# Kernel optimization log

Hardware: AMD Instinct MI355X
Metric: run time of the kernel (lower is better)

Reference implementation:

```python
import jax, jax.numpy as jnp
import numpy as np

B = 2097152
CXR, ECG, EHR = 15, 14, 13
TOTAL = CXR + ECG + EHR  # 42
LN_EPS = 1e-5


def setup_inputs() -> dict:
    key = jax.random.key(0)
    ks = jax.random.split(key, 40)
    f32 = jnp.float32
    inp = {
        "cxr_probs": jax.random.normal(ks[0], (B, CXR), dtype=f32),
        "ecg_probs": jax.random.normal(ks[1], (B, ECG), dtype=f32),
        "ehr_probs": jax.random.normal(ks[2], (B, EHR), dtype=f32),
    }
    for i, (name, E) in enumerate([("cxr", CXR), ("ecg", ECG), ("ehr", EHR)]):
        k0 = 3 + i * 8
        s_in = 1.0 / np.sqrt(E)
        s_kv = 1.0 / np.sqrt(TOTAL)
        inp[f"in_w_{name}"] = jax.random.normal(ks[k0], (3 * E, E), dtype=f32) * s_in
        inp[f"in_b_{name}"] = jnp.zeros((3 * E,), dtype=f32)
        inp[f"out_w_{name}"] = jax.random.normal(ks[k0 + 1], (E, E), dtype=f32) * s_in
        inp[f"out_b_{name}"] = jnp.zeros((E,), dtype=f32)
        inp[f"kv_w_{name}"] = jax.random.normal(ks[k0 + 2], (E, TOTAL), dtype=f32) * s_kv
        inp[f"kv_b_{name}"] = jax.random.normal(ks[k0 + 3], (E,), dtype=f32) * s_kv
        inp[f"ln_g_{name}"] = jnp.ones((E,), dtype=f32)
        inp[f"ln_b_{name}"] = jnp.zeros((E,), dtype=f32)
    return inp


def _branch(x, ctx, in_w, in_b, out_w, out_b, kv_w, kv_b, ln_g, ln_b):
    # x: [B, E], ctx: [B, 42]
    E = x.shape[-1]
    kv = ctx @ kv_w.T + kv_b                      # [B, E]
    # nn.MultiheadAttention with q_len = kv_len = 1: softmax over a single
    # key is identically 1, so attn_out == v_proj(kv) exactly.
    Wv, bv = in_w[2 * E:], in_b[2 * E:]
    v = kv @ Wv.T + bv                            # [B, E]
    attended = v @ out_w.T + out_b                # [B, E]
    y = x + attended
    mu = jnp.mean(y, axis=-1, keepdims=True)
    var = jnp.mean(jnp.square(y - mu), axis=-1, keepdims=True)
    return (y - mu) * jax.lax.rsqrt(var + LN_EPS) * ln_g + ln_b


def reference(cxr_probs, ecg_probs, ehr_probs,
              in_w_cxr, in_b_cxr, out_w_cxr, out_b_cxr, kv_w_cxr, kv_b_cxr, ln_g_cxr, ln_b_cxr,
              in_w_ecg, in_b_ecg, out_w_ecg, out_b_ecg, kv_w_ecg, kv_b_ecg, ln_g_ecg, ln_b_ecg,
              in_w_ehr, in_b_ehr, out_w_ehr, out_b_ehr, kv_w_ehr, kv_b_ehr, ln_g_ehr, ln_b_ehr):
    ctx = jnp.concatenate([cxr_probs, ecg_probs, ehr_probs], axis=1)  # [B, 42]
    cxr_out = _branch(cxr_probs, ctx, in_w_cxr, in_b_cxr, out_w_cxr, out_b_cxr,
                      kv_w_cxr, kv_b_cxr, ln_g_cxr, ln_b_cxr)
    ecg_out = _branch(ecg_probs, ctx, in_w_ecg, in_b_ecg, out_w_ecg, out_b_ecg,
                      kv_w_ecg, kv_b_ecg, ln_g_ecg, ln_b_ecg)
    ehr_out = _branch(ehr_probs, ctx, in_w_ehr, in_b_ehr, out_w_ehr, out_b_ehr,
                      kv_w_ehr, kv_b_ehr, ln_g_ehr, ln_b_ehr)
    return (cxr_out, ecg_out, ehr_out)
```

## Files before the change

### kernel.cpp

```cpp
#include <hip/hip_runtime.h>
#include <stdint.h>

constexpr int CXR = 15, ECG = 14, EHR = 13;
constexpr int TOTAL = 42;
constexpr int MPITCH = 44;
constexpr float LN_EPS = 1e-5f;

constexpr int WS_M    = 0;
constexpr int WS_B    = TOTAL * MPITCH;
constexpr int WS_G    = WS_B + TOTAL;
constexpr int WS_BETA = WS_G + TOTAL;
constexpr int WS_FRAG = 1976;

constexpr int WROWS = 64;
constexpr int ARENA_B = 11264;
constexpr int S0F = 0, S1F = WROWS * CXR, S2F = S1F + WROWS * ECG;
constexpr int WC0 = WROWS * CXR / 4, WC1 = WROWS * ECG / 4, WC2 = WROWS * EHR / 4;

typedef _Float16 half8 __attribute__((ext_vector_type(8)));
typedef float float4v __attribute__((ext_vector_type(4)));
typedef __attribute__((address_space(4))) const float CFc;
__device__ __forceinline__ CFc* cast1(const float* p) {
    return (CFc*)(unsigned long long)p;
}

struct FuseArgs {
    const float *in_w, *in_b, *out_w, *out_b, *kv_w, *kv_b, *ln_g, *ln_b;
    int E, R;
};

__global__ void fuse_weights_kernel(FuseArgs a0, FuseArgs a1, FuseArgs a2,
                                    float* __restrict__ ws) {
    FuseArgs a = (blockIdx.x == 0) ? a0 : (blockIdx.x == 1 ? a1 : a2);
    const int E = a.E, R = a.R;
    const int tid = threadIdx.x;

    __shared__ float T1[15 * 42];
    __shared__ float b1[15];

    for (int idx = tid; idx < E * TOTAL; idx += blockDim.x) {
        int i = idx / TOTAL, j = idx % TOTAL;
        float acc = 0.f;
        for (int k = 0; k < E; ++k)
            acc = fmaf(a.in_w[(2 * E + i) * E + k], a.kv_w[k * TOTAL + j], acc);
        T1[i * TOTAL + j] = acc;
    }
    if (tid < E) {
        float acc = a.in_b[2 * E + tid];
        for (int k = 0; k < E; ++k)
            acc = fmaf(a.in_w[(2 * E + tid) * E + k], a.kv_b[k], acc);
        b1[tid] = acc;
    }
    __syncthreads();

    for (int idx = tid; idx < E * MPITCH; idx += blockDim.x) {
        int i = idx / MPITCH, j = idx % MPITCH;
        float acc = 0.f;
        if (j < TOTAL)
            for (int k = 0; k < E; ++k)
                acc = fmaf(a.out_w[i * E + k], T1[k * TOTAL + j], acc);
        ws[WS_M + (R + i) * MPITCH + j] = acc;
    }
    if (tid < E) {
        float acc = a.out_b[tid];
        for (int k = 0; k < E; ++k)
            acc = fmaf(a.out_w[tid * E + k], b1[k], acc);
        ws[WS_B + R + tid]    = acc;
        ws[WS_G + R + tid]    = a.ln_g[tid];
        ws[WS_BETA + R + tid] = a.ln_b[tid];
    }
}

__global__ void fuse_frags_kernel(float* __restrict__ ws) {
    const int tid = threadIdx.x;
    if (tid >= 384) return;
    const int l = tid & 63, nt = tid >> 6;
    const int n = nt >> 1, t = nt & 1;
    const int col = n * 16 + (l & 15);
    const int k0 = t * 32 + 8 * (l >> 4);
    half8 h;
#pragma unroll
    for (int i = 0; i < 8; ++i) {
        int k = k0 + i;
        float v = 0.f;
        if (col < TOTAL) {
            if (k < TOTAL) {
                v = ws[WS_M + col * MPITCH + k];
                if (k == col) v += 1.f;
            } else if (k == TOTAL) {
                v = ws[WS_B + col];
            }
        }
        h[i] = (_Float16)v;
    }
    ((half8*)(ws + WS_FRAG))[nt * 64 + l] = h;
}

template <int CH>
__device__ __forceinline__ void stage_wave(const float* __restrict__ g,
                                           float* lds_seg_base, int lane) {
#pragma unroll
    for (int it = 0; it < (CH + 63) / 64; ++it) {
        int idx = lane + it * 64;
        if (idx < CH) {
            const __attribute__((address_space(1))) void* src =
                (const __attribute__((address_space(1))) void*)
                    ((const char*)g + (size_t)idx * 16);
            __attribute__((address_space(3))) void* dst =
                (__attribute__((address_space(3))) void*)
                    ((char*)lds_seg_base + it * 1024);
            __builtin_amdgcn_global_load_lds(src, dst, 16, 0, 0);
        }
    }
}

__global__ __launch_bounds__(128) void cmca_main(
        const float* __restrict__ cxr, const float* __restrict__ ecg,
        const float* __restrict__ ehr, const float* __restrict__ ws,
        float* __restrict__ out_cxr, float* __restrict__ out_ecg,
        float* __restrict__ out_ehr) {
    __shared__ __align__(16) char smem[2 * ARENA_B];
    const int tid = threadIdx.x;
    const int w = tid >> 6, lane = tid & 63;
    char* arena = smem + w * ARENA_B;
    float* af = (float*)arena;
    const size_t gw = (size_t)blockIdx.x * 2 + w;

    const half8* fr = (const half8*)(ws + WS_FRAG);
    half8 bfrag[6];
#pragma unroll
    for (int q = 0; q < 6; ++q) bfrag[q] = fr[q * 64 + lane];

    stage_wave<WC0>(cxr + gw * (size_t)(WROWS * CXR), af + S0F, lane);
    stage_wave<WC1>(ecg + gw * (size_t)(WROWS * ECG), af + S1F, lane);
    stage_wave<WC2>(ehr + gw * (size_t)(WROWS * EHR), af + S2F, lane);
    asm volatile("s_waitcnt vmcnt(0)" ::: "memory");

    float x[TOTAL];
#pragma unroll
    for (int j = 0; j < CXR; ++j) x[j] = af[S0F + lane * CXR + j];
#pragma unroll
    for (int j = 0; j < ECG; ++j) x[CXR + j] = af[S1F + lane * ECG + j];
#pragma unroll
    for (int j = 0; j < EHR; ++j) x[CXR + ECG + j] = af[S2F + lane * EHR + j];
    __builtin_amdgcn_sched_barrier(0);

    {
        const int swz = (lane & 7) << 4;
#pragma unroll
        for (int j = 0; j < 8; ++j) {
            half8 h;
#pragma unroll
            for (int e = 0; e < 8; ++e) {
                int idx = j * 8 + e;
                float v = (idx < TOTAL) ? x[idx] : (idx == TOTAL ? 1.f : 0.f);
                h[e] = (_Float16)v;
            }
            *(half8*)(arena + ((lane * 128 + j * 16) ^ swz)) = h;
        }
    }
    __builtin_amdgcn_sched_barrier(0);

    half8 afr[4][2];
#pragma unroll
    for (int m = 0; m < 4; ++m) {
        int row = m * 16 + (lane & 15);
        int rswz = (row & 7) << 4;
#pragma unroll
        for (int t = 0; t < 2; ++t)
            afr[m][t] = *(const half8*)(arena +
                ((row * 128 + t * 64 + (lane >> 4) * 16) ^ rswz));
    }
    __builtin_amdgcn_sched_barrier(0);

    float4v acc[4][3];
#pragma unroll
    for (int m = 0; m < 4; ++m)
#pragma unroll
        for (int n = 0; n < 3; ++n) acc[m][n] = float4v{0.f, 0.f, 0.f, 0.f};
#pragma unroll
    for (int t = 0; t < 2; ++t)
#pragma unroll
        for (int m = 0; m < 4; ++m)
#pragma unroll
            for (int n = 0; n < 3; ++n)
                acc[m][n] = __builtin_amdgcn_mfma_f32_16x16x32_f16(
                    afr[m][t], bfrag[n * 2 + t], acc[m][n], 0, 0, 0);

    __builtin_amdgcn_sched_barrier(0);
#pragma unroll
    for (int m = 0; m < 4; ++m)
#pragma unroll
        for (int n = 0; n < 3; ++n)
#pragma unroll
            for (int r = 0; r < 4; ++r) {
                int row = m * 16 + (lane >> 4) * 4 + r;
                int col = n * 16 + (lane & 15);
                if (col < MPITCH) af[row * MPITCH + col] = acc[m][n][r];
            }
    __builtin_amdgcn_sched_barrier(0);

    float y[MPITCH];
#pragma unroll
    for (int j = 0; j < 11; ++j) {
        float4v q = *(const float4v*)(af + lane * MPITCH + j * 4);
        y[j * 4 + 0] = q[0]; y[j * 4 + 1] = q[1];
        y[j * 4 + 2] = q[2]; y[j * 4 + 3] = q[3];
    }
    __builtin_amdgcn_sched_barrier(0);

    float res[TOTAL];
    {
#define LN_SEG(S, E)                                                       \
        {                                                                  \
            float mu = 0.f;                                                \
            _Pragma("unroll")                                              \
            for (int i = 0; i < (E); ++i) mu += y[(S) + i];                \
            mu *= (1.0f / (E));                                            \
            float var = 0.f;                                               \
            _Pragma("unroll")                                              \
            for (int i = 0; i < (E); ++i) {                                \
                float d = y[(S) + i] - mu; var = fmaf(d, d, var);          \
            }                                                              \
            var *= (1.0f / (E));                                           \
            float rs = rsqrtf(var + LN_EPS);                               \
            _Pragma("unroll")                                              \
            for (int i = 0; i < (E); ++i) {                                \
                float nv = (y[(S) + i] - mu) * rs;                         \
                res[(S) + i] = fmaf(nv, *cast1(ws + WS_G + (S) + i),       \
                                    *cast1(ws + WS_BETA + (S) + i));       \
            }                                                              \
        }
        LN_SEG(0, CXR)
        LN_SEG(CXR, ECG)
        LN_SEG(CXR + ECG, EHR)
#undef LN_SEG
    }
#pragma unroll
    for (int j = 0; j < CXR; ++j) af[S0F + lane * CXR + j] = res[j];
#pragma unroll
    for (int j = 0; j < ECG; ++j) af[S1F + lane * ECG + j] = res[CXR + j];
#pragma unroll
    for (int j = 0; j < EHR; ++j) af[S2F + lane * EHR + j] = res[CXR + ECG + j];
    __builtin_amdgcn_sched_barrier(0);

    const float4v* wb4 = (const float4v*)af;
    float4v* o0 = (float4v*)(out_cxr + gw * (size_t)(WROWS * CXR));
    float4v* o1 = (float4v*)(out_ecg + gw * (size_t)(WROWS * ECG));
    float4v* o2 = (float4v*)(out_ehr + gw * (size_t)(WROWS * EHR));
#pragma unroll
    for (int it = 0; it < 4; ++it) {
        int idx = lane + it * 64;
        if (idx < WC0) o0[idx] = wb4[idx];
    }
#pragma unroll
    for (int it = 0; it < 4; ++it) {
        int idx = lane + it * 64;
        if (idx < WC1) o1[idx] = wb4[WC0 + idx];
    }
#pragma unroll
    for (int it = 0; it < 4; ++it) {
        int idx = lane + it * 64;
        if (idx < WC2) o2[idx] = wb4[WC0 + WC1 + idx];
    }
}

extern "C" void kernel_launch(void* const* d_in, const int* in_sizes, int n_in,
                              void* d_out, int out_size, void* d_ws, size_t ws_size,
                              hipStream_t stream) {
    const float* cxr = (const float*)d_in[0];
    const float* ecg = (const float*)d_in[1];
    const float* ehr = (const float*)d_in[2];
    float* ws = (float*)d_ws;
    float* out = (float*)d_out;

    const size_t Bn = (size_t)in_sizes[0] / CXR;

    auto mk = [&](int base, int E, int R) {
        FuseArgs a;
        a.in_w  = (const float*)d_in[base + 0];
        a.in_b  = (const float*)d_in[base + 1];
        a.out_w = (const float*)d_in[base + 2];
        a.out_b = (const float*)d_in[base + 3];
        a.kv_w  = (const float*)d_in[base + 4];
        a.kv_b  = (const float*)d_in[base + 5];
        a.ln_g  = (const float*)d_in[base + 6];
        a.ln_b  = (const float*)d_in[base + 7];
        a.E = E; a.R = R;
        return a;
    };
    FuseArgs a0 = mk(3, CXR, 0);
    FuseArgs a1 = mk(11, ECG, CXR);
    FuseArgs a2 = mk(19, EHR, CXR + ECG);

    fuse_weights_kernel<<<3, 256, 0, stream>>>(a0, a1, a2, ws);
    fuse_frags_kernel<<<1, 384, 0, stream>>>(ws);

    const int nblocks = (int)(Bn / (WROWS * 2));
    cmca_main<<<nblocks, 128, 0, stream>>>(cxr, ecg, ehr, ws,
                                           out,
                                           out + Bn * CXR,
                                           out + Bn * (CXR + ECG));
}
```

Before: 146.5 us.

## Persistent single-wave blocks with prefetch double-buffering and in-register LayerNorm

Replaces one-shot two-wave blocks with a persistent grid of single-wave blocks that loop over 64-row tiles. While the current tile is computed, the next tile is prefetched into LDS via global_load_lds. The GEMM is transposed so weights act as the A operand, letting LayerNorm run on MFMA accumulators with cross-lane shuffles instead of an LDS round trip. Costs include the fixed grid size, reliance on a hand-tuned vmcnt wait count for correctness, and possibly lower occupancy from the larger LDS arena.

```diff
diff --git a/kernel.cpp b/kernel.cpp
--- a/kernel.cpp
+++ b/kernel.cpp
@@ -13,16 +13,16 @@
 constexpr int WS_FRAG = 1976;
 
 constexpr int WROWS = 64;
-constexpr int ARENA_B = 11264;
 constexpr int S0F = 0, S1F = WROWS * CXR, S2F = S1F + WROWS * ECG;
 constexpr int WC0 = WROWS * CXR / 4, WC1 = WROWS * ECG / 4, WC2 = WROWS * EHR / 4;
+constexpr int STAGE_B = WROWS * TOTAL * 4;
+constexpr int WORK_B  = WROWS * TOTAL * 4;
+constexpr int ARENA_B = STAGE_B + WORK_B;
+
+constexpr int GRID_BLOCKS = 1792;
 
 typedef _Float16 half8 __attribute__((ext_vector_type(8)));
 typedef float float4v __attribute__((ext_vector_type(4)));
-typedef __attribute__((address_space(4))) const float CFc;
-__device__ __forceinline__ CFc* cast1(const float* p) {
-    return (CFc*)(unsigned long long)p;
-}
 
 struct FuseArgs {
     const float *in_w, *in_b, *out_w, *out_b, *kv_w, *kv_b, *ln_g, *ln_b;
@@ -75,20 +75,23 @@
     const int tid = threadIdx.x;
     if (tid >= 384) return;
     const int l = tid & 63, nt = tid >> 6;
-    const int n = nt >> 1, t = nt & 1;
-    const int col = n * 16 + (l & 15);
+    const int m = nt >> 1, t = nt & 1;
+    const int j = l & 15;
     const int k0 = t * 32 + 8 * (l >> 4);
+    const int offm = (m == 0) ? 0 : (m == 1 ? CXR : CXR + ECG);
+    const int Em   = (m == 0) ? CXR : (m == 1 ? ECG : EHR);
     half8 h;
 #pragma unroll
     for (int i = 0; i < 8; ++i) {
         int k = k0 + i;
         float v = 0.f;
-        if (col < TOTAL) {
+        if (j < Em) {
+            int glob = offm + j;
             if (k < TOTAL) {
-                v = ws[WS_M + col * MPITCH + k];
-                if (k == col) v += 1.f;
+                v = ws[WS_M + glob * MPITCH + k];
+                if (k == glob) v += 1.f;
             } else if (k == TOTAL) {
-                v = ws[WS_B + col];
+                v = ws[WS_B + glob];
             }
         }
         h[i] = (_Float16)v;
@@ -97,8 +100,8 @@
 }
 
 template <int CH>
-__device__ __forceinline__ void stage_wave(const float* __restrict__ g,
-                                           float* lds_seg_base, int lane) {
+__device__ __forceinline__ void stage_seg(const float* __restrict__ g,
+                                          float* lds_seg_base, int lane) {
 #pragma unroll
     for (int it = 0; it < (CH + 63) / 64; ++it) {
         int idx = lane + it * 64;
@@ -114,154 +117,162 @@
     }
 }
 
-__global__ __launch_bounds__(128) void cmca_main(
+__global__ __launch_bounds__(64) void cmca_main(
         const float* __restrict__ cxr, const float* __restrict__ ecg,
         const float* __restrict__ ehr, const float* __restrict__ ws,
         float* __restrict__ out_cxr, float* __restrict__ out_ecg,
-        float* __restrict__ out_ehr) {
-    __shared__ __align__(16) char smem[2 * ARENA_B];
-    const int tid = threadIdx.x;
-    const int w = tid >> 6, lane = tid & 63;
-    char* arena = smem + w * ARENA_B;
-    float* af = (float*)arena;
-    const size_t gw = (size_t)blockIdx.x * 2 + w;
+        float* __restrict__ out_ehr, int NT) {
+    __shared__ __align__(16) char arena[ARENA_B];
+    float* stg = (float*)arena;
+    char*  fb  = arena + STAGE_B;
+    float* wk  = (float*)(arena + STAGE_B);
+
+    const int lane = threadIdx.x;
+    const int h = lane >> 4, b15 = lane & 15;
 
     const half8* fr = (const half8*)(ws + WS_FRAG);
-    half8 bfrag[6];
-#pragma unroll
-    for (int q = 0; q < 6; ++q) bfrag[q] = fr[q * 64 + lane];
-
-    stage_wave<WC0>(cxr + gw * (size_t)(WROWS * CXR), af + S0F, lane);
-    stage_wave<WC1>(ecg + gw * (size_t)(WROWS * ECG), af + S1F, lane);
-    stage_wave<WC2>(ehr + gw * (size_t)(WROWS * EHR), af + S2F, lane);
+    half8 wf[3][2];
+#pragma unroll
+    for (int m = 0; m < 3; ++m)
+#pragma unroll
+        for (int t = 0; t < 2; ++t) wf[m][t] = fr[(m * 2 + t) * 64 + lane];
+
+    constexpr int Earr[3]  = {CXR, ECG, EHR};
+    constexpr int OFFa[3]  = {0, CXR, CXR + ECG};
+    float gg[3][4], bb[3][4];
+#pragma unroll
+    for (int m = 0; m < 3; ++m)
+#pragma unroll
+        for (int r = 0; r < 4; ++r) {
+            int j = 4 * h + r;
+            bool v = j < Earr[m];
+            gg[m][r] = v ? ws[WS_G + OFFa[m] + j] : 0.f;
+            bb[m][r] = v ? ws[WS_BETA + OFFa[m] + j] : 0.f;
+        }
+
+    const int t0 = blockIdx.x;
+    stage_seg<WC0>(cxr + (size_t)t0 * (WROWS * CXR), stg + S0F, lane);
+    stage_seg<WC1>(ecg + (size_t)t0 * (WROWS * ECG), stg + S1F, lane);
+    stage_seg<WC2>(ehr + (size_t)t0 * (WROWS * EHR), stg + S2F, lane);
     asm volatile("s_waitcnt vmcnt(0)" ::: "memory");
 
-    float x[TOTAL];
-#pragma unroll
-    for (int j = 0; j < CXR; ++j) x[j] = af[S0F + lane * CXR + j];
-#pragma unroll
-    for (int j = 0; j < ECG; ++j) x[CXR + j] = af[S1F + lane * ECG + j];
-#pragma unroll
-    for (int j = 0; j < EHR; ++j) x[CXR + ECG + j] = af[S2F + lane * EHR + j];
-    __builtin_amdgcn_sched_barrier(0);
-
-    {
+    for (int t = t0; t < NT; t += GRID_BLOCKS) {
+        float x[TOTAL];
+#pragma unroll
+        for (int j = 0; j < CXR; ++j) x[j] = stg[S0F + lane * CXR + j];
+#pragma unroll
+        for (int j = 0; j < ECG; ++j) x[CXR + j] = stg[S1F + lane * ECG + j];
+#pragma unroll
+        for (int j = 0; j < EHR; ++j) x[CXR + ECG + j] = stg[S2F + lane * EHR + j];
+        asm volatile("s_waitcnt lgkmcnt(0)" ::: "memory");
+        __builtin_amdgcn_sched_barrier(0);
+
+        const int tn = t + GRID_BLOCKS;
+        const bool more = tn < NT;
+        if (more) {
+            stage_seg<WC0>(cxr + (size_t)tn * (WROWS * CXR), stg + S0F, lane);
+            stage_seg<WC1>(ecg + (size_t)tn * (WROWS * ECG), stg + S1F, lane);
+            stage_seg<WC2>(ehr + (size_t)tn * (WROWS * EHR), stg + S2F, lane);
+        }
+
         const int swz = (lane & 7) << 4;
 #pragma unroll
-        for (int j = 0; j < 8; ++j) {
-            half8 h;
+        for (int j = 0; j < 6; ++j) {
+            half8 h8;
 #pragma unroll
             for (int e = 0; e < 8; ++e) {
-                int idx = j * 8 + e;
-                float v = (idx < TOTAL) ? x[idx] : (idx == TOTAL ? 1.f : 0.f);
-                h[e] = (_Float16)v;
+                int k = j * 8 + e;
+                float v = (k < TOTAL) ? x[k] : (k == TOTAL ? 1.f : 0.f);
+                h8[e] = (_Float16)v;
             }
-            *(half8*)(arena + ((lane * 128 + j * 16) ^ swz)) = h;
-        }
-    }
-    __builtin_amdgcn_sched_barrier(0);
-
-    half8 afr[4][2];
-#pragma unroll
-    for (int m = 0; m < 4; ++m) {
-        int row = m * 16 + (lane & 15);
-        int rswz = (row & 7) << 4;
-#pragma unroll
-        for (int t = 0; t < 2; ++t)
-            afr[m][t] = *(const half8*)(arena +
-                ((row * 128 + t * 64 + (lane >> 4) * 16) ^ rswz));
-    }
-    __builtin_amdgcn_sched_barrier(0);
-
-    float4v acc[4][3];
-#pragma unroll
-    for (int m = 0; m < 4; ++m)
-#pragma unroll
-        for (int n = 0; n < 3; ++n) acc[m][n] = float4v{0.f, 0.f, 0.f, 0.f};
-#pragma unroll
-    for (int t = 0; t < 2; ++t)
-#pragma unroll
-        for (int m = 0; m < 4; ++m)
-#pragma unroll
-            for (int n = 0; n < 3; ++n)
-                acc[m][n] = __builtin_amdgcn_mfma_f32_16x16x32_f16(
-                    afr[m][t], bfrag[n * 2 + t], acc[m][n], 0, 0, 0);
-
-    __builtin_amdgcn_sched_barrier(0);
-#pragma unroll
-    for (int m = 0; m < 4; ++m)
-#pragma unroll
-        for (int n = 0; n < 3; ++n)
-#pragma unroll
-            for (int r = 0; r < 4; ++r) {
-                int row = m * 16 + (lane >> 4) * 4 + r;
-                int col = n * 16 + (lane & 15);
-                if (col < MPITCH) af[row * MPITCH + col] = acc[m][n][r];
+            *(half8*)(fb + lane * 128 + ((j * 16) ^ swz)) = h8;
+        }
+        *(float4v*)(fb + lane * 128 + (96 ^ swz))  = float4v{0.f, 0.f, 0.f, 0.f};
+        *(float4v*)(fb + lane * 128 + (112 ^ swz)) = float4v{0.f, 0.f, 0.f, 0.f};
+
+        half8 xf[4][2];
+#pragma unroll
+        for (int n = 0; n < 4; ++n) {
+            int row = n * 16 + b15;
+            int rsw = (row & 7) << 4;
+#pragma unroll
+            for (int t2 = 0; t2 < 2; ++t2)
+                xf[n][t2] = *(const half8*)(fb + row * 128 +
+                                            ((t2 * 64 + h * 16) ^ rsw));
+        }
+
+        float4v acc[3][4];
+#pragma unroll
+        for (int m = 0; m < 3; ++m)
+#pragma unroll
+            for (int n = 0; n < 4; ++n) acc[m][n] = float4v{0.f, 0.f, 0.f, 0.f};
+#pragma unroll
+        for (int t2 = 0; t2 < 2; ++t2)
+#pragma unroll
+            for (int m = 0; m < 3; ++m)
+#pragma unroll
+                for (int n = 0; n < 4; ++n)
+                    acc[m][n] = __builtin_amdgcn_mfma_f32_16x16x32_f16(
+                        wf[m][t2], xf[n][t2], acc[m][n], 0, 0, 0);
+
+#pragma unroll
+        for (int n = 0; n < 4; ++n) {
+            int brow = n * 16 + b15;
+#pragma unroll
+            for (int m = 0; m < 3; ++m) {
+                constexpr int SEGF[3] = {S0F, S1F, S2F};
+                const int E = Earr[m];
+                const float invE = 1.0f / E;
+                const float PAD = (float)(16 - E);
+                float s = acc[m][n][0] + acc[m][n][1] + acc[m][n][2] + acc[m][n][3];
+                s += __shfl_xor(s, 16, 64);
+                s += __shfl_xor(s, 32, 64);
+                float mu = s * invE;
+                float q = 0.f;
+#pragma unroll
+                for (int r = 0; r < 4; ++r) {
+                    float d = acc[m][n][r] - mu;
+                    q = fmaf(d, d, q);
+                }
+                q += __shfl_xor(q, 16, 64);
+                q += __shfl_xor(q, 32, 64);
+                float var = (q - PAD * mu * mu) * invE;
+                float rs = rsqrtf(var + LN_EPS);
+#pragma unroll
+                for (int r = 0; r < 4; ++r) {
+                    int j = 4 * h + r;
+                    if (j < E) {
+                        float nv = (acc[m][n][r] - mu) * rs;
+                        wk[SEGF[m] + brow * E + j] = fmaf(nv, gg[m][r], bb[m][r]);
+                    }
+                }
             }
-    __builtin_amdgcn_sched_barrier(0);
-
-    float y[MPITCH];
-#pragma unroll
-    for (int j = 0; j < 11; ++j) {
-        float4v q = *(const float4v*)(af + lane * MPITCH + j * 4);
-        y[j * 4 + 0] = q[0]; y[j * 4 + 1] = q[1];
-        y[j * 4 + 2] = q[2]; y[j * 4 + 3] = q[3];
-    }
-    __builtin_amdgcn_sched_barrier(0);
-
-    float res[TOTAL];
-    {
-#define LN_SEG(S, E)                                                       \
-        {                                                                  \
-            float mu = 0.f;                                                \
-            _Pragma("unroll")                                              \
-            for (int i = 0; i < (E); ++i) mu += y[(S) + i];                \
-            mu *= (1.0f / (E));                                            \
-            float var = 0.f;                                               \
-            _Pragma("unroll")                                              \
-            for (int i = 0; i < (E); ++i) {                                \
-                float d = y[(S) + i] - mu; var = fmaf(d, d, var);          \
-            }                                                              \
-            var *= (1.0f / (E));                                           \
-            float rs = rsqrtf(var + LN_EPS);                               \
-            _Pragma("unroll")                                              \
-            for (int i = 0; i < (E); ++i) {                                \
-                float nv = (y[(S) + i] - mu) * rs;                         \
-                res[(S) + i] = fmaf(nv, *cast1(ws + WS_G + (S) + i),       \
-                                    *cast1(ws + WS_BETA + (S) + i));       \
-            }                                                              \
-        }
-        LN_SEG(0, CXR)
-        LN_SEG(CXR, ECG)
-        LN_SEG(CXR + ECG, EHR)
-#undef LN_SEG
-    }
-#pragma unroll
-    for (int j = 0; j < CXR; ++j) af[S0F + lane * CXR + j] = res[j];
-#pragma unroll
-    for (int j = 0; j < ECG; ++j) af[S1F + lane * ECG + j] = res[CXR + j];
-#pragma unroll
-    for (int j = 0; j < EHR; ++j) af[S2F + lane * EHR + j] = res[CXR + ECG + j];
-    __builtin_amdgcn_sched_barrier(0);
-
-    const float4v* wb4 = (const float4v*)af;
-    float4v* o0 = (float4v*)(out_cxr + gw * (size_t)(WROWS * CXR));
-    float4v* o1 = (float4v*)(out_ecg + gw * (size_t)(WROWS * ECG));
-    float4v* o2 = (float4v*)(out_ehr + gw * (size_t)(WROWS * EHR));
-#pragma unroll
-    for (int it = 0; it < 4; ++it) {
-        int idx = lane + it * 64;
-        if (idx < WC0) o0[idx] = wb4[idx];
-    }
-#pragma unroll
-    for (int it = 0; it < 4; ++it) {
-        int idx = lane + it * 64;
-        if (idx < WC1) o1[idx] = wb4[WC0 + idx];
-    }
-#pragma unroll
-    for (int it = 0; it < 4; ++it) {
-        int idx = lane + it * 64;
-        if (idx < WC2) o2[idx] = wb4[WC0 + WC1 + idx];
+        }
+
+        const float4v* w4 = (const float4v*)wk;
+        float4v* o0 = (float4v*)(out_cxr + (size_t)t * (WROWS * CXR));
+        float4v* o1 = (float4v*)(out_ecg + (size_t)t * (WROWS * ECG));
+        float4v* o2 = (float4v*)(out_ehr + (size_t)t * (WROWS * EHR));
+#pragma unroll
+        for (int it = 0; it < 4; ++it) {
+            int idx = lane + it * 64;
+            if (idx < WC0) o0[idx] = w4[idx];
+        }
+#pragma unroll
+        for (int it = 0; it < 4; ++it) {
+            int idx = lane + it * 64;
+            if (idx < WC1) o1[idx] = w4[WC0 + idx];
+        }
+#pragma unroll
+        for (int it = 0; it < 4; ++it) {
+            int idx = lane + it * 64;
+            if (idx < WC2) o2[idx] = w4[WC0 + WC1 + idx];
+        }
+
+        if (more) {
+            asm volatile("s_waitcnt vmcnt(12)" ::: "memory");
+            __builtin_amdgcn_sched_barrier(0);
+        }
     }
 }
 
@@ -296,9 +307,9 @@
     fuse_weights_kernel<<<3, 256, 0, stream>>>(a0, a1, a2, ws);
     fuse_frags_kernel<<<1, 384, 0, stream>>>(ws);
 
-    const int nblocks = (int)(Bn / (WROWS * 2));
-    cmca_main<<<nblocks, 128, 0, stream>>>(cxr, ecg, ehr, ws,
-                                           out,
-                                           out + Bn * CXR,
-                                           out + Bn * (CXR + ECG));
-}
+    const int NT = (int)(Bn / WROWS);
+    cmca_main<<<GRID_BLOCKS, 64, 0, stream>>>(cxr, ecg, ehr, ws,
+                                              out,
+                                              out + Bn * CXR,
+                                              out + Bn * (CXR + ECG), NT);
+}
```

New measurement: 162.2 us. 1.11x slower.
